# Kernel tuning notes

Hardware: AMD Instinct MI355X
Metric: run time of the kernel (lower is better)

Reference implementation:

```python
import jax, jax.numpy as jnp
import numpy as np

N_NODES = 50000
N_EDGES = 1600000
IN_DIM, HID_DIM, OUT_DIM = 512, 128, 16


def spmm(edge_src, edge_dst, edge_vals, x):
    # sparse.mm(A, x): out[dst] += A[dst, src] * x[src]
    msgs = edge_vals[:, None] * x[edge_src]  # [E, D]
    return jax.ops.segment_sum(msgs, edge_dst, num_segments=N_NODES)


def setup_inputs() -> dict:
    key = jax.random.key(0)
    k1, k2, k3, k4, k5, k6 = jax.random.split(key, 6)
    feature = jax.random.normal(k1, (N_NODES, IN_DIM), dtype=jnp.float32)
    edge_src = jax.random.randint(k2, (N_EDGES,), 0, N_NODES, dtype=jnp.int32)
    edge_dst = jax.random.randint(k3, (N_EDGES,), 0, N_NODES, dtype=jnp.int32)
    edge_vals = jax.random.uniform(k4, (N_EDGES,), dtype=jnp.float32)
    # kaiming_uniform-style init: bound = sqrt(6 / fan_in) (a=sqrt(5) omitted for simplicity of scale)
    b1 = float(np.sqrt(6.0 / IN_DIM))
    b2 = float(np.sqrt(6.0 / HID_DIM))
    W1 = jax.random.uniform(k5, (IN_DIM, HID_DIM), dtype=jnp.float32, minval=-b1, maxval=b1)
    W2 = jax.random.uniform(k6, (HID_DIM, OUT_DIM), dtype=jnp.float32, minval=-b2, maxval=b2)
    return {"feature": feature, "edge_src": edge_src, "edge_dst": edge_dst,
            "edge_vals": edge_vals, "W1": W1, "W2": W2}


def reference(feature, edge_src, edge_dst, edge_vals, W1, W2):
    # layer 1: dense matmul -> sparse aggregation -> ReLU
    h = jax.nn.relu(spmm(edge_src, edge_dst, edge_vals, feature @ W1))
    # layer 2
    out = spmm(edge_src, edge_dst, edge_vals, h @ W2)
    return out
```

## Files before the change

### kernel.cpp

```cpp
#include <hip/hip_runtime.h>

#define N_NODES 50000
#define N_EDGES 1600000
#define IN_DIM 512
#define HID_DIM 128
#define OUT_DIM 16

#define BKT_SHIFT 6
#define BKT_NODES 64
#define NB ((N_NODES + BKT_NODES - 1) / BKT_NODES)
#define SC_EDGES 8192
#define SC_BLOCKS ((N_EDGES + SC_EDGES - 1) / SC_EDGES)
#define PREP_BLOCKS ((IN_DIM * HID_DIM + 1023) / 1024)
#define NS_CAP 2560
#define MG_GEMM_BLOCKS ((N_NODES + 127) / 128)

typedef __attribute__((ext_vector_type(8))) __bf16 bf16x8;
typedef __attribute__((ext_vector_type(4))) __bf16 bf16x4;
typedef __attribute__((ext_vector_type(8))) unsigned short ushort8;
typedef __attribute__((ext_vector_type(4))) float f32x4;
typedef __attribute__((ext_vector_type(2))) float f32x2;

static __device__ __forceinline__ unsigned short f2bf(float x) {
    unsigned int u = __float_as_uint(x);
    u += 0x7FFFu + ((u >> 16) & 1u);
    return (unsigned short)(u >> 16);
}
static __device__ __forceinline__ float bf2f(unsigned short v) {
    return __uint_as_float(((unsigned int)v) << 16);
}
static __device__ __forceinline__ unsigned char f2fp8(float x) {
    int pk = __builtin_amdgcn_cvt_pk_fp8_f32(x, x, 0, false);
    return (unsigned char)(pk & 0xFF);
}

__device__ inline int wave_incl_scan(int v) {
    #pragma unroll
    for (int off = 1; off < 64; off <<= 1) {
        int x = __shfl_up(v, off, 64);
        if ((threadIdx.x & 63) >= off) v += x;
    }
    return v;
}


__global__ void zero_bcnt_kernel(int* __restrict__ bcnt) {
    int t = threadIdx.x;
    if (t < NB) bcnt[t] = 0;
}

__global__ __launch_bounds__(1024) void hist_prep_kernel(const int* __restrict__ dst,
                                                         int* __restrict__ bcnt,
                                                         int* __restrict__ blk_hist_T,
                                                         const float* __restrict__ W1,
                                                         unsigned short* __restrict__ Wt) {
    if (blockIdx.x >= SC_BLOCKS) {
        int i = (blockIdx.x - SC_BLOCKS) * 1024 + threadIdx.x;
        if (i < IN_DIM * HID_DIM) {
            int k = i >> 7, col = i & 127;
            Wt[(size_t)col * IN_DIM + k] = f2bf(W1[i]);
        }
        return;
    }
    __shared__ int lc[NB];
    const int t = threadIdx.x;
    for (int b = t; b < NB; b += 1024) lc[b] = 0;
    __syncthreads();
    const int eb = blockIdx.x * SC_EDGES + t * 8;
    #pragma unroll
    for (int q = 0; q < 2; q++) {
        int e0 = eb + q * 4;
        if (e0 + 4 <= N_EDGES) {
            int4 d4 = *(const int4*)&dst[e0];
            atomicAdd(&lc[d4.x >> BKT_SHIFT], 1);
            atomicAdd(&lc[d4.y >> BKT_SHIFT], 1);
            atomicAdd(&lc[d4.z >> BKT_SHIFT], 1);
            atomicAdd(&lc[d4.w >> BKT_SHIFT], 1);
        } else {
            for (int k = 0; k < 4; k++) {
                int e = e0 + k;
                if (e < N_EDGES) atomicAdd(&lc[dst[e] >> BKT_SHIFT], 1);
            }
        }
    }
    __syncthreads();
    for (int b = t; b < NB; b += 1024) {
        int c = lc[b];
        blk_hist_T[(size_t)b * SC_BLOCKS + blockIdx.x] = c;
        if (c) atomicAdd(&bcnt[b], c);
    }
}

__global__ __launch_bounds__(1024) void bucket_scan_kernel(const int* __restrict__ bcnt,
                                                           int* __restrict__ bucket_ptr) {
    __shared__ int wsums[16];
    const int t = threadIdx.x;
    const int lane = t & 63, wid = t >> 6;
    int v = (t < NB) ? bcnt[t] : 0;
    int incl = wave_incl_scan(v);
    if (lane == 63) wsums[wid] = incl;
    __syncthreads();
    if (wid == 0) {
        int wv = (lane < 16) ? wsums[lane] : 0;
        int ws = wave_incl_scan(wv);
        if (lane < 16) wsums[lane] = ws;
    }
    __syncthreads();
    int woff = wid ? wsums[wid - 1] : 0;
    int excl = woff + incl - v;
    if (t < NB) bucket_ptr[t] = excl;
    if (t == NB - 1) bucket_ptr[NB] = excl + v;
}

__global__ __launch_bounds__(512) void base_scan_kernel(const int* __restrict__ bucket_ptr,
                                                        int* __restrict__ blk_hist_T) {
    const int lane = threadIdx.x & 63;
    const int b = blockIdx.x * 8 + (threadIdx.x >> 6);
    if (b >= NB) return;
    int* row = blk_hist_T + (size_t)b * SC_BLOCKS;
    int carry = bucket_ptr[b];
    for (int c0 = 0; c0 < SC_BLOCKS; c0 += 64) {
        int idx = c0 + lane;
        int v = (idx < SC_BLOCKS) ? row[idx] : 0;
        int incl = wave_incl_scan(v);
        if (idx < SC_BLOCKS) row[idx] = carry + incl - v;
        carry += __shfl(incl, 63, 64);
    }
}


#define G1_XSTR 72
#define G1_BSTR 72
__global__ __launch_bounds__(512) void scatter_gemm1_kernel(const float* __restrict__ X,
                                                            const unsigned short* __restrict__ Wt,
                                                            unsigned char* __restrict__ h0,
                                                            const int* __restrict__ src,
                                                            const int* __restrict__ dst,
                                                            const float* __restrict__ val,
                                                            const int* __restrict__ blk_hist_T,
                                                            int2* __restrict__ pairs_bkt) {
    if (blockIdx.x < MG_GEMM_BLOCKS) {
        __shared__ __align__(16) unsigned short Xs[128 * G1_XSTR];
        __shared__ __align__(16) unsigned short Bs[128 * G1_BSTR];
        const int t = threadIdx.x;
        const int lane = t & 63;
        const int wave = t >> 6;
        const int wr = wave >> 2;
        const int wc = wave & 3;
        const int c = lane & 15, g = lane >> 4;
        const int m0 = blockIdx.x * 128;

        f32x4 acc[4][2];
        #pragma unroll
        for (int mt = 0; mt < 4; mt++)
            #pragma unroll
            for (int nt = 0; nt < 2; nt++) acc[mt][nt] = (f32x4){0.f, 0.f, 0.f, 0.f};

        float4 xrA[4], xrB[4];
        ushort8 brA[2], brB[2];

        #define G1_LOAD(XR, BR, kt)                                                          \
            _Pragma("unroll")                                                                \
            for (int p = 0; p < 4; p++) {                                                    \
                int idx = p * 512 + t;                                                       \
                int xrow = idx >> 4, xseg = idx & 15;                                        \
                int grow = m0 + xrow; grow = (grow < N_NODES) ? grow : (N_NODES - 1);        \
                XR[p] = *(const float4*)&X[(size_t)grow * IN_DIM + (kt) * 64 + xseg * 4];    \
            }                                                                                \
            _Pragma("unroll")                                                                \
            for (int p = 0; p < 2; p++) {                                                    \
                int idx = p * 512 + t;                                                       \
                int bcol = idx >> 3, bseg = idx & 7;                                         \
                BR[p] = *(const ushort8*)&Wt[(size_t)bcol * IN_DIM + (kt) * 64 + bseg * 8];  \
            }

        #define G1_WRITE(XR, BR)                                                             \
            _Pragma("unroll")                                                                \
            for (int p = 0; p < 4; p++) {                                                    \
                int idx = p * 512 + t;                                                       \
                int xrow = idx >> 4, xseg = idx & 15;                                        \
                bf16x4 xw;                                                                   \
                xw[0] = (__bf16)XR[p].x; xw[1] = (__bf16)XR[p].y;                            \
                xw[2] = (__bf16)XR[p].z; xw[3] = (__bf16)XR[p].w;                            \
                *(bf16x4*)&Xs[xrow * G1_XSTR + xseg * 4] = xw;                               \
            }                                                                                \
            _Pragma("unroll")                                                                \
            for (int p = 0; p < 2; p++) {                                                    \
                int idx = p * 512 + t;                                                       \
                int bcol = idx >> 3, bseg = idx & 7;                                         \
                *(ushort8*)&Bs[bcol * G1_BSTR + bseg * 8] = BR[p];                           \
            }

        G1_LOAD(xrA, brA, 0)
        G1_LOAD(xrB, brB, 1)
        #pragma unroll
        for (int kt = 0; kt < 8; kt++) {
            if (kt & 1) { G1_WRITE(xrB, brB) } else { G1_WRITE(xrA, brA) }
            __syncthreads();
            if (kt + 2 < 8) {
                if (kt & 1) { G1_LOAD(xrB, brB, kt + 2) } else { G1_LOAD(xrA, brA, kt + 2) }
            }
            #pragma unroll
            for (int ks = 0; ks < 2; ks++) {
                bf16x8 bf[2];
                #pragma unroll
                for (int nt = 0; nt < 2; nt++) {
                    int col = wc * 32 + nt * 16 + c;
                    bf[nt] = *(const bf16x8*)&Bs[col * G1_BSTR + ks * 32 + g * 8];
                }
                #pragma unroll
                for (int mt = 0; mt < 4; mt++) {
                    bf16x8 af = *(const bf16x8*)&Xs[(wr * 64 + mt * 16 + c) * G1_XSTR + ks * 32 + g * 8];
                    #pragma unroll
                    for (int nt = 0; nt < 2; nt++)
                        acc[mt][nt] = __builtin_amdgcn_mfma_f32_16x16x32_bf16(af, bf[nt],
                                                                              acc[mt][nt], 0, 0, 0);
                }
            }
            __syncthreads();
        }
        #undef G1_LOAD
        #undef G1_WRITE

        #pragma unroll
        for (int mt = 0; mt < 4; mt++) {
            #pragma unroll
            for (int r = 0; r < 4; r++) {
                int row = m0 + wr * 64 + mt * 16 + g * 4 + r;
                if (row < N_NODES) {
                    #pragma unroll
                    for (int nt = 0; nt < 2; nt++) {
                        int col = wc * 32 + nt * 16 + c;
                        h0[(size_t)row * HID_DIM + col] = f2fp8(acc[mt][nt][r]);
                    }
                }
            }
        }
    } else {
        __shared__ int cbase[NB];
        const int sb = blockIdx.x - MG_GEMM_BLOCKS;
        const int t = threadIdx.x;
        for (int b = t; b < NB; b += 512)
            cbase[b] = blk_hist_T[(size_t)b * SC_BLOCKS + sb];
        __syncthreads();
        const int eb = sb * SC_EDGES + t * 16;
        #pragma unroll
        for (int q = 0; q < 4; q++) {
            int e0 = eb + q * 4;
            if (e0 + 4 <= N_EDGES) {
                int4 s4 = *(const int4*)&src[e0];
                int4 d4 = *(const int4*)&dst[e0];
                float4 v4 = *(const float4*)&val[e0];
                #pragma unroll
                for (int k = 0; k < 4; k++) {
                    int ss = (k == 0) ? s4.x : (k == 1) ? s4.y : (k == 2) ? s4.z : s4.w;
                    int dd = (k == 0) ? d4.x : (k == 1) ? d4.y : (k == 2) ? d4.z : d4.w;
                    float vv = (k == 0) ? v4.x : (k == 1) ? v4.y : (k == 2) ? v4.z : v4.w;
                    int b = dd >> BKT_SHIFT, dl = dd & (BKT_NODES - 1);
                    int pos = atomicAdd(&cbase[b], 1);
                    int2 pr;
                    pr.x = ss | (dl << 16);
                    pr.y = __float_as_int(vv);
                    pairs_bkt[pos] = pr;
                }
            } else {
                for (int k = 0; k < 4; k++) {
                    int e = e0 + k;
                    if (e < N_EDGES) {
                        int dd = dst[e];
                        int b = dd >> BKT_SHIFT, dl = dd & (BKT_NODES - 1);
                        int pos = atomicAdd(&cbase[b], 1);
                        int2 pr;
                        pr.x = src[e] | (dl << 16);
                        pr.y = __float_as_int(val[e]);
                        pairs_bkt[pos] = pr;
                    }
                }
            }
        }
    }
}

__global__ __launch_bounds__(512) void node_sort_fused_kernel(const int2* __restrict__ pairs_bkt,
                                                              const int* __restrict__ bucket_ptr,
                                                              int* __restrict__ row_ptr,
                                                              int2* __restrict__ pairs) {
    __shared__ int cnt[BKT_NODES];
    __shared__ int base[BKT_NODES];
    __shared__ int2 stage[NS_CAP];
    const int t = threadIdx.x;
    const int b = blockIdx.x;
    const int s = bucket_ptr[b], e = bucket_ptr[b + 1];
    if (t < BKT_NODES) cnt[t] = 0;
    __syncthreads();
    for (int i = s + t; i < e; i += 512)
        atomicAdd(&cnt[pairs_bkt[i].x >> 16], 1);
    __syncthreads();
    if (t < BKT_NODES) {
        int v = cnt[t];
        int incl = wave_incl_scan(v);
        base[t] = s + incl - v;
    }
    __syncthreads();
    if (t < BKT_NODES) {
        int n = b * BKT_NODES + t;
        if (n < N_NODES) row_ptr[n] = base[t];
        cnt[t] = 0;
    }
    if (b == NB - 1 && t == 0) row_ptr[N_NODES] = N_EDGES;
    __syncthreads();
    for (int i = s + t; i < e; i += 512) {
        int2 pr = pairs_bkt[i];
        int dl = pr.x >> 16;
        int p = base[dl] + atomicAdd(&cnt[dl], 1);
        int loc = p - s;
        if (loc < NS_CAP) stage[loc] = pr;
        else pairs[p] = pr;
    }
    __syncthreads();
    const int lim = min(e - s, NS_CAP);
    for (int j = t; j < lim; j += 512)
        pairs[s + j] = stage[j];
}


__global__ __launch_bounds__(256) void spmm1_fused_kernel(const unsigned char* __restrict__ h0,
                                                          const int* __restrict__ row_ptr,
                                                          const int2* __restrict__ pairs,
                                                          const float* __restrict__ W2,
                                                          unsigned short* __restrict__ h2) {
    __shared__ float W2s[HID_DIM][OUT_DIM];
    __shared__ float h_lds[4][HID_DIM];
    const int t = threadIdx.x;
    #pragma unroll
    for (int p = 0; p < 8; p++) {
        int idx = p * 256 + t;
        W2s[idx >> 4][idx & 15] = W2[idx];
    }

    const int wid = __builtin_amdgcn_readfirstlane(t >> 6);
    const int n = blockIdx.x * 4 + wid;
    const int lane = t & 63;
    const int s = row_ptr[n], e = row_ptr[n + 1];
    const unsigned char* h0l = h0 + lane * 2;
    float ax = 0.f, ay = 0.f;
    for (int base = s; base < e; base += 8) {
        float vv[8];
        const unsigned char* rp[8];
        #pragma unroll
        for (int k = 0; k < 8; k++) {
            int idx = base + k;
            int cidx = (idx < e) ? idx : (e - 1);
            int2 pr = pairs[cidx];
            vv[k] = (idx < e) ? __int_as_float(pr.y) : 0.f;
            rp[k] = h0l + (size_t)(pr.x & 0xFFFF) * HID_DIM;
        }
        unsigned short gg[8];
        #pragma unroll
        for (int k = 0; k < 8; k++) gg[k] = *(const unsigned short*)rp[k];
        #pragma unroll
        for (int k = 0; k < 8; k++) {
            f32x2 f = __builtin_amdgcn_cvt_pk_f32_fp8((int)gg[k], false);
            ax += vv[k] * f.x;
            ay += vv[k] * f.y;
        }
    }
    f32x2 hw;
    hw.x = fmaxf(ax, 0.f);
    hw.y = fmaxf(ay, 0.f);
    *(f32x2*)&h_lds[wid][lane * 2] = hw;
    __syncthreads();

    const int node = t >> 6;
    const int j = (t & 63) >> 2;
    const int q = t & 3;
    const float* hr = h_lds[node];
    float p = 0.f;
    #pragma unroll
    for (int kk = 0; kk < 32; kk++) {
        int k = q * 32 + kk;
        p += hr[k] * W2s[k][j];
    }
    p += __shfl_xor(p, 1, 64);
    p += __shfl_xor(p, 2, 64);
    if (q == 0) {
        int nn = blockIdx.x * 4 + node;
        h2[(size_t)nn * OUT_DIM + j] = f2bf(p);
    }
}

__global__ __launch_bounds__(256) void spmm2_node_kernel(const unsigned short* __restrict__ h2,
                                                         const int* __restrict__ row_ptr,
                                                         const int2* __restrict__ pairs,
                                                         float* __restrict__ out) {
    const int idx = blockIdx.x * 256 + threadIdx.x;
    const int n = idx >> 4;
    const int d = idx & 15;
    if (n >= N_NODES) return;
    const int s = row_ptr[n], e = row_ptr[n + 1];
    float acc = 0.f;
    for (int base = s; base < e; base += 8) {
        float vv[8];
        const unsigned short* gp[8];
        #pragma unroll
        for (int k = 0; k < 8; k++) {
            int i = base + k;
            int ci = (i < e) ? i : (e - 1);
            int2 pr = pairs[ci];
            vv[k] = (i < e) ? __int_as_float(pr.y) : 0.f;
            gp[k] = h2 + (size_t)(pr.x & 0xFFFF) * OUT_DIM + d;
        }
        unsigned short gg[8];
        #pragma unroll
        for (int k = 0; k < 8; k++) gg[k] = *gp[k];
        #pragma unroll
        for (int k = 0; k < 8; k++) acc += vv[k] * bf2f(gg[k]);
    }
    out[(size_t)n * OUT_DIM + d] = acc;
}


extern "C" void kernel_launch(void* const* d_in, const int* in_sizes, int n_in,
                              void* d_out, int out_size, void* d_ws, size_t ws_size,
                              hipStream_t stream) {
    const float* feature   = (const float*)d_in[0];
    const int*   edge_src  = (const int*)d_in[1];
    const int*   edge_dst  = (const int*)d_in[2];
    const float* edge_vals = (const float*)d_in[3];
    const float* W1        = (const float*)d_in[4];
    const float* W2        = (const float*)d_in[5];
    float* out = (float*)d_out;

    char* ws = (char*)d_ws;
    size_t off = 0;
    auto alloc = [&](size_t bytes) {
        void* p = ws + off;
        off += (bytes + 255) & ~(size_t)255;
        return p;
    };
    unsigned char*  h0    = (unsigned char*)alloc((size_t)N_NODES * HID_DIM);
    unsigned short* Wt    = (unsigned short*)alloc((size_t)IN_DIM * HID_DIM * 2);
    unsigned short* h2    = (unsigned short*)alloc((size_t)N_NODES * OUT_DIM * 2);
    int*   bcnt           = (int*)alloc((size_t)NB * 4);
    int*   bucket_ptr     = (int*)alloc((size_t)(NB + 1) * 4);
    int*   blk_hist_T     = (int*)alloc((size_t)NB * SC_BLOCKS * 4);
    int*   row_ptr        = (int*)alloc((size_t)(N_NODES + 1) * 4);
    int2*  pairs_bkt      = (int2*)alloc((size_t)N_EDGES * 8);
    int2*  pairs          = (int2*)alloc((size_t)N_EDGES * 8);

    zero_bcnt_kernel<<<1, 1024, 0, stream>>>(bcnt);
    hist_prep_kernel<<<SC_BLOCKS + PREP_BLOCKS, 1024, 0, stream>>>(edge_dst, bcnt, blk_hist_T,
                                                                   W1, Wt);
    bucket_scan_kernel<<<1, 1024, 0, stream>>>(bcnt, bucket_ptr);
    base_scan_kernel<<<(NB + 7) / 8, 512, 0, stream>>>(bucket_ptr, blk_hist_T);
    scatter_gemm1_kernel<<<MG_GEMM_BLOCKS + SC_BLOCKS, 512, 0, stream>>>(
        feature, Wt, h0, edge_src, edge_dst, edge_vals, blk_hist_T, pairs_bkt);
    node_sort_fused_kernel<<<NB, 512, 0, stream>>>(pairs_bkt, bucket_ptr, row_ptr, pairs);

    spmm1_fused_kernel<<<(N_NODES + 3) / 4, 256, 0, stream>>>(h0, row_ptr, pairs, W2, h2);
    spmm2_node_kernel<<<(N_NODES * 16 + 255) / 256, 256, 0, stream>>>(h2, row_ptr, pairs, out);
}
```

Measured before the change: 134.2 us.

## Load GEMM1 tiles directly to LDS with XOR-swizzled layout, convert at read

Replaces the register-staged, double-buffered global-to-LDS copy of the X and W tiles with direct global_load_lds transfers into XOR-swizzled shared memory. X is now kept as fp32 in LDS and converted to bf16 when fragments are read for MFMA. This removes the register staging and the conversion-on-write. In exchange the LDS footprint for X doubles, and the prefetch overlap shrinks to single buffering, because the next tile is issued only after the compute and the barrier.

```diff
diff --git a/kernel.cpp b/kernel.cpp
--- a/kernel.cpp
+++ b/kernel.cpp
@@ -32,6 +32,11 @@
 static __device__ __forceinline__ unsigned char f2fp8(float x) {
     int pk = __builtin_amdgcn_cvt_pk_fp8_f32(x, x, 0, false);
     return (unsigned char)(pk & 0xFF);
+}
+static __device__ __forceinline__ void gload_lds16(const void* g, void* l) {
+    __builtin_amdgcn_global_load_lds(
+        (const __attribute__((address_space(1))) unsigned int*)g,
+        (__attribute__((address_space(3))) unsigned int*)l, 16, 0, 0);
 }
 
 __device__ inline int wave_incl_scan(int v) {
@@ -129,8 +134,6 @@
 }
 
 
-#define G1_XSTR 72
-#define G1_BSTR 72
 __global__ __launch_bounds__(512) void scatter_gemm1_kernel(const float* __restrict__ X,
                                                             const unsigned short* __restrict__ Wt,
                                                             unsigned char* __restrict__ h0,
@@ -140,8 +143,8 @@
                                                             const int* __restrict__ blk_hist_T,
                                                             int2* __restrict__ pairs_bkt) {
     if (blockIdx.x < MG_GEMM_BLOCKS) {
-        __shared__ __align__(16) unsigned short Xs[128 * G1_XSTR];
-        __shared__ __align__(16) unsigned short Bs[128 * G1_BSTR];
+        __shared__ __align__(16) float Xs[128 * 64];
+        __shared__ __align__(16) unsigned short Bs[128 * 64];
         const int t = threadIdx.x;
         const int lane = t & 63;
         const int wave = t >> 6;
@@ -156,71 +159,58 @@
             #pragma unroll
             for (int nt = 0; nt < 2; nt++) acc[mt][nt] = (f32x4){0.f, 0.f, 0.f, 0.f};
 
-        float4 xrA[4], xrB[4];
-        ushort8 brA[2], brB[2];
-
-        #define G1_LOAD(XR, BR, kt)                                                          \
-            _Pragma("unroll")                                                                \
-            for (int p = 0; p < 4; p++) {                                                    \
-                int idx = p * 512 + t;                                                       \
-                int xrow = idx >> 4, xseg = idx & 15;                                        \
-                int grow = m0 + xrow; grow = (grow < N_NODES) ? grow : (N_NODES - 1);        \
-                XR[p] = *(const float4*)&X[(size_t)grow * IN_DIM + (kt) * 64 + xseg * 4];    \
-            }                                                                                \
-            _Pragma("unroll")                                                                \
-            for (int p = 0; p < 2; p++) {                                                    \
-                int idx = p * 512 + t;                                                       \
-                int bcol = idx >> 3, bseg = idx & 7;                                         \
-                BR[p] = *(const ushort8*)&Wt[(size_t)bcol * IN_DIM + (kt) * 64 + bseg * 8];  \
+        #define G1_ISSUE(kt)                                                             \
+            _Pragma("unroll")                                                            \
+            for (int s4 = 0; s4 < 4; s4++) {                                             \
+                int cc = s4 * 512 + t;                                                   \
+                int xrow = cc >> 4;                                                      \
+                int xcs = (cc & 15) ^ (xrow & 15);                                       \
+                int grow = m0 + xrow; grow = (grow < N_NODES) ? grow : (N_NODES - 1);    \
+                gload_lds16(&X[(size_t)grow * IN_DIM + (kt) * 64 + xcs * 4],             \
+                            (char*)Xs + s4 * 8192 + wave * 1024);                        \
+            }                                                                            \
+            _Pragma("unroll")                                                            \
+            for (int s4 = 0; s4 < 2; s4++) {                                             \
+                int cc = s4 * 512 + t;                                                   \
+                int bcol = cc >> 3;                                                      \
+                int bcs = (cc & 7) ^ (bcol & 7);                                         \
+                gload_lds16(&Wt[(size_t)bcol * IN_DIM + (kt) * 64 + bcs * 8],            \
+                            (char*)Bs + s4 * 8192 + wave * 1024);                        \
             }
 
-        #define G1_WRITE(XR, BR)                                                             \
-            _Pragma("unroll")                                                                \
-            for (int p = 0; p < 4; p++) {                                                    \
-                int idx = p * 512 + t;                                                       \
-                int xrow = idx >> 4, xseg = idx & 15;                                        \
-                bf16x4 xw;                                                                   \
-                xw[0] = (__bf16)XR[p].x; xw[1] = (__bf16)XR[p].y;                            \
-                xw[2] = (__bf16)XR[p].z; xw[3] = (__bf16)XR[p].w;                            \
-                *(bf16x4*)&Xs[xrow * G1_XSTR + xseg * 4] = xw;                               \
-            }                                                                                \
-            _Pragma("unroll")                                                                \
-            for (int p = 0; p < 2; p++) {                                                    \
-                int idx = p * 512 + t;                                                       \
-                int bcol = idx >> 3, bseg = idx & 7;                                         \
-                *(ushort8*)&Bs[bcol * G1_BSTR + bseg * 8] = BR[p];                           \
-            }
-
-        G1_LOAD(xrA, brA, 0)
-        G1_LOAD(xrB, brB, 1)
-        #pragma unroll
+        G1_ISSUE(0)
         for (int kt = 0; kt < 8; kt++) {
-            if (kt & 1) { G1_WRITE(xrB, brB) } else { G1_WRITE(xrA, brA) }
             __syncthreads();
-            if (kt + 2 < 8) {
-                if (kt & 1) { G1_LOAD(xrB, brB, kt + 2) } else { G1_LOAD(xrA, brA, kt + 2) }
-            }
             #pragma unroll
             for (int ks = 0; ks < 2; ks++) {
-                bf16x8 bf[2];
+                bf16x8 bfr[2];
                 #pragma unroll
                 for (int nt = 0; nt < 2; nt++) {
                     int col = wc * 32 + nt * 16 + c;
-                    bf[nt] = *(const bf16x8*)&Bs[col * G1_BSTR + ks * 32 + g * 8];
+                    int slot = (ks * 4 + g) ^ (col & 7);
+                    bfr[nt] = *(const bf16x8*)&Bs[col * 64 + slot * 8];
                 }
                 #pragma unroll
                 for (int mt = 0; mt < 4; mt++) {
-                    bf16x8 af = *(const bf16x8*)&Xs[(wr * 64 + mt * 16 + c) * G1_XSTR + ks * 32 + g * 8];
+                    int r = wr * 64 + mt * 16 + c;
+                    int q = ks * 8 + g * 2;
+                    f32x4 a0 = *(const f32x4*)&Xs[r * 64 + ((q ^ (r & 15)) * 4)];
+                    f32x4 a1 = *(const f32x4*)&Xs[r * 64 + (((q + 1) ^ (r & 15)) * 4)];
+                    bf16x8 af;
+                    af[0] = (__bf16)a0[0]; af[1] = (__bf16)a0[1];
+                    af[2] = (__bf16)a0[2]; af[3] = (__bf16)a0[3];
+                    af[4] = (__bf16)a1[0]; af[5] = (__bf16)a1[1];
+                    af[6] = (__bf16)a1[2]; af[7] = (__bf16)a1[3];
                     #pragma unroll
                     for (int nt = 0; nt < 2; nt++)
-                        acc[mt][nt] = __builtin_amdgcn_mfma_f32_16x16x32_bf16(af, bf[nt],
+                        acc[mt][nt] = __builtin_amdgcn_mfma_f32_16x16x32_bf16(af, bfr[nt],
                                                                               acc[mt][nt], 0, 0, 0);
                 }
             }
             __syncthreads();
-        }
-        #undef G1_LOAD
-        #undef G1_WRITE
+            if (kt < 7) G1_ISSUE(kt + 1)
+        }
+        #undef G1_ISSUE
 
         #pragma unroll
         for (int mt = 0; mt < 4; mt++) {
```

Measured after the change: 135.6 us. No clear change (+1.0%).
